# Kernel optimization log

Measured on AMD Instinct MI355X. Metric: run time of the kernel, lower is better.

## Reference

```python
import jax, jax.numpy as jnp
import numpy as np

N = 50000      # nodes per graph
E = 800000     # edges per graph
IN_DIM = 64
HIDDEN = 128
OUT_DIM = 2
P = 100000     # candidate residue pairs


def setup_inputs() -> dict:
    key = jax.random.key(0)
    ks = jax.random.split(key, 12)
    x1 = jax.random.normal(ks[0], (N, IN_DIM), dtype=jnp.float32)
    x2 = jax.random.normal(ks[1], (N, IN_DIM), dtype=jnp.float32)
    edge_index1 = jax.random.randint(ks[2], (2, E), 0, N, dtype=jnp.int64)
    edge_index2 = jax.random.randint(ks[3], (2, E), 0, N, dtype=jnp.int64)
    label = jax.random.randint(ks[4], (P, 2), 0, N, dtype=jnp.int64)
    s = 0.05
    W0 = jax.random.normal(ks[5], (IN_DIM, HIDDEN), dtype=jnp.float32) * s
    W1 = jax.random.normal(ks[6], (HIDDEN, HIDDEN), dtype=jnp.float32) * s
    W2 = jax.random.normal(ks[7], (HIDDEN, HIDDEN), dtype=jnp.float32) * s
    b0 = jnp.zeros((HIDDEN,), dtype=jnp.float32)
    b1 = jnp.zeros((HIDDEN,), dtype=jnp.float32)
    b2 = jnp.zeros((HIDDEN,), dtype=jnp.float32)
    fcW = jax.random.normal(ks[8], (2 * HIDDEN, OUT_DIM), dtype=jnp.float32) * s
    fcb = jnp.zeros((OUT_DIM,), dtype=jnp.float32)
    return {"x1": x1, "edge_index1": edge_index1, "x2": x2,
            "edge_index2": edge_index2, "label": label,
            "W0": W0, "b0": b0, "W1": W1, "b1": b1, "W2": W2, "b2": b2,
            "fcW": fcW, "fcb": fcb}


def gcn_conv(x, src, dst, W, b):
    """PyG GCNConv: linear, add self-loops, symmetric D^-1/2 (A+I) D^-1/2 aggregation."""
    n = x.shape[0]
    h = x @ W                                   # [n, out]
    loops = jnp.arange(n, dtype=src.dtype)
    src_sl = jnp.concatenate([src, loops])      # [E+n]
    dst_sl = jnp.concatenate([dst, loops])
    deg = jax.ops.segment_sum(jnp.ones_like(src_sl, dtype=h.dtype), dst_sl,
                              num_segments=n)
    dinv = jax.lax.rsqrt(jnp.maximum(deg, 1.0e-12))
    norm = dinv[src_sl] * dinv[dst_sl]          # [E+n]
    msgs = h[src_sl] * norm[:, None]            # gather + scale
    out = jax.ops.segment_sum(msgs, dst_sl, num_segments=n)  # scatter-add
    return out + b


def gcn_tower(x, edge_index, params):
    src, dst = edge_index[0], edge_index[1]
    for (W, b) in params:
        x = jax.nn.relu(gcn_conv(x, src, dst, W, b))
    return x


def reference(x1, edge_index1, x2, edge_index2, label,
              W0, b0, W1, b1, W2, b2, fcW, fcb):
    params = [(W0, b0), (W1, b1), (W2, b2)]
    x_ligand = gcn_tower(x1, edge_index1, params)    # shared GCN weights
    x_receptor = gcn_tower(x2, edge_index2, params)
    x = jnp.concatenate([x_ligand[label[:, 0]], x_receptor[label[:, 1]]], axis=1)
    return jax.nn.relu(x @ fcW + fcb)
```

## Files before the change

### kernel.cpp

```cpp
#include <hip/hip_runtime.h>
#include <math.h>

typedef __attribute__((ext_vector_type(8))) short bf16x8;
typedef __attribute__((ext_vector_type(4))) float f32x4;

__device__ inline unsigned short f2bf(float f) {
    unsigned int u = __float_as_uint(f);
    unsigned int r = u + 0x7fffu + ((u >> 16) & 1u);
    return (unsigned short)(r >> 16);
}
__device__ inline float bf2f(unsigned short b) {
    return __uint_as_float(((unsigned int)b) << 16);
}


__global__ void histU_kernel(const int* __restrict__ d1, const int* __restrict__ d2,
                             int* __restrict__ cnt, int E, int N) {
    int i = blockIdx.x * blockDim.x + threadIdx.x;
    if (i < E) atomicAdd(&cnt[d1[i]], 1);
    else if (i < 2 * E) atomicAdd(&cnt[N + d2[i - E]], 1);
}

__global__ __launch_bounds__(256) void block_reduce_kernel(const int* __restrict__ cnt,
                                                           float* __restrict__ dinv,
                                                           int* __restrict__ blockSums, int NN) {
    int i = blockIdx.x * 256 + threadIdx.x;
    int v = 0;
    if (i < NN) {
        v = cnt[i];
        dinv[i] = 1.0f / sqrtf((float)(v + 1));
    }
    int s = v;
#pragma unroll
    for (int o = 32; o; o >>= 1) s += __shfl_down(s, o);
    __shared__ int ws[4];
    if ((threadIdx.x & 63) == 0) ws[threadIdx.x >> 6] = s;
    __syncthreads();
    if (threadIdx.x == 0) blockSums[blockIdx.x] = ws[0] + ws[1] + ws[2] + ws[3];
}

__global__ __launch_bounds__(1024) void scan_sums_kernel(const int* __restrict__ blockSums,
                                                         int* __restrict__ blockOff, int nb,
                                                         int* __restrict__ rowptr, int NN) {
    __shared__ int sh[1024];
    int t = threadIdx.x;
    int v = (t < nb) ? blockSums[t] : 0;
    sh[t] = v;
    __syncthreads();
    for (int o = 1; o < 1024; o <<= 1) {
        int u = (t >= o) ? sh[t - o] : 0;
        __syncthreads();
        sh[t] += u;
        __syncthreads();
    }
    if (t < nb) blockOff[t] = sh[t] - v;
    if (t == 1023) rowptr[NN] = sh[1023];
}

__global__ __launch_bounds__(256) void scan_write_kernel(const int* __restrict__ cnt,
                                                         const int* __restrict__ blockOff,
                                                         int* __restrict__ rowptr, int NN) {
    __shared__ int sh[256];
    int i = blockIdx.x * 256 + threadIdx.x;
    int t = threadIdx.x;
    int v = (i < NN) ? cnt[i] : 0;
    sh[t] = v;
    __syncthreads();
    for (int o = 1; o < 256; o <<= 1) {
        int u = (t >= o) ? sh[t - o] : 0;
        __syncthreads();
        sh[t] += u;
        __syncthreads();
    }
    if (i < NN) rowptr[i] = blockOff[blockIdx.x] + sh[t] - v;
}

__global__ void placeU_kernel(const int* __restrict__ s1, const int* __restrict__ d1,
                              const int* __restrict__ s2, const int* __restrict__ d2,
                              const int* __restrict__ rowptr, int* __restrict__ cnt,
                              int* __restrict__ csr, int E, int N) {
    int i = blockIdx.x * blockDim.x + threadIdx.x;
    int s, d;
    if (i < E)          { s = s1[i];         d = d1[i]; }
    else if (i < 2 * E) { s = s2[i - E] + N; d = d2[i - E] + N; }
    else return;
    int p = atomicSub(&cnt[d], 1);
    csr[rowptr[d] + p - 1] = s;
}


__global__ void prep_weights(const float* __restrict__ W0, const float* __restrict__ W1,
                             const float* __restrict__ W2,
                             unsigned short* __restrict__ W0h, unsigned short* __restrict__ W0l,
                             unsigned short* __restrict__ W1h, unsigned short* __restrict__ W1l,
                             unsigned short* __restrict__ W2h, unsigned short* __restrict__ W2l) {
    const float* W; unsigned short *Wh, *Wl; int K;
    if (blockIdx.x == 0)      { W = W0; Wh = W0h; Wl = W0l; K = 64; }
    else if (blockIdx.x == 1) { W = W1; Wh = W1h; Wl = W1l; K = 128; }
    else                      { W = W2; Wh = W2h; Wl = W2l; K = 128; }
    for (int i = threadIdx.x; i < K * 128; i += 256) {
        int k = i >> 7, c = i & 127;
        float v = W[i];
        unsigned short h = f2bf(v);
        unsigned short l = f2bf(v - bf2f(h));
        Wh[c * K + k] = h;
        Wl[c * K + k] = l;
    }
}


__global__ void prescale_kernel(const float* __restrict__ x1, const float* __restrict__ x2,
                                const float* __restrict__ dinv, float* __restrict__ X0, int NN,
                                int N) {
    int i = blockIdx.x * blockDim.x + threadIdx.x;
    if (i >= NN * 16) return;
    int r = i >> 4;
    const float4* src = (r < N) ? (const float4*)(x1) + i
                                : (const float4*)(x2) + (i - N * 16);
    float4 v = *src;
    float d = dinv[r];
    v.x *= d; v.y *= d; v.z *= d; v.w *= d;
    reinterpret_cast<float4*>(X0)[i] = v;
}


__global__ void agg64_kernel(const float* __restrict__ X0, const int* __restrict__ rowptr,
                             const int* __restrict__ csr,
                             unsigned short* __restrict__ Shi, unsigned short* __restrict__ Slo,
                             int NN) {
    int w = blockIdx.x * (blockDim.x >> 6) + (threadIdx.x >> 6);
    int lane = threadIdx.x & 63;
    if (w >= NN) return;
    int beg = rowptr[w], end = rowptr[w + 1];
    float acc = X0[(size_t)w * 64 + lane];
    int e = beg;
    int full_end = beg + ((end - beg) & ~7);
    for (; e < full_end; e += 8) {
        int s0 = csr[e], s1 = csr[e + 1], s2 = csr[e + 2], s3 = csr[e + 3];
        int s4 = csr[e + 4], s5 = csr[e + 5], s6 = csr[e + 6], s7 = csr[e + 7];
        float v0 = X0[(size_t)s0 * 64 + lane];
        float v1 = X0[(size_t)s1 * 64 + lane];
        float v2 = X0[(size_t)s2 * 64 + lane];
        float v3 = X0[(size_t)s3 * 64 + lane];
        float v4 = X0[(size_t)s4 * 64 + lane];
        float v5 = X0[(size_t)s5 * 64 + lane];
        float v6 = X0[(size_t)s6 * 64 + lane];
        float v7 = X0[(size_t)s7 * 64 + lane];
        acc += ((v0 + v1) + (v2 + v3)) + ((v4 + v5) + (v6 + v7));
    }
    if (e < end) {
#pragma unroll
        for (int j = 0; j < 7; ++j) {
            int a = e + j;
            bool vld = a < end;
            int s = csr[vld ? a : beg];
            float m = vld ? 1.f : 0.f;
            acc += m * X0[(size_t)s * 64 + lane];
        }
    }
    unsigned short h = f2bf(acc);
    Shi[(size_t)w * 64 + lane] = h;
    Slo[(size_t)w * 64 + lane] = f2bf(acc - bf2f(h));
}


__global__ void agg128_kernel(const float* __restrict__ Xf, const int* __restrict__ rowptr,
                              const int* __restrict__ csr,
                              unsigned short* __restrict__ Shi, unsigned short* __restrict__ Slo,
                              int NN) {
    int w = blockIdx.x * (blockDim.x >> 6) + (threadIdx.x >> 6);
    int lane = threadIdx.x & 63;
    if (w >= NN) return;
    const float2* X = (const float2*)Xf;
    int beg = rowptr[w], end = rowptr[w + 1];
    float2 self = X[(size_t)w * 64 + lane];
    float ax = self.x, ay = self.y;
    int e = beg;
    int full_end = beg + ((end - beg) & ~7);
    for (; e < full_end; e += 8) {
        int s0 = csr[e], s1 = csr[e + 1], s2 = csr[e + 2], s3 = csr[e + 3];
        int s4 = csr[e + 4], s5 = csr[e + 5], s6 = csr[e + 6], s7 = csr[e + 7];
        float2 v0 = X[(size_t)s0 * 64 + lane];
        float2 v1 = X[(size_t)s1 * 64 + lane];
        float2 v2 = X[(size_t)s2 * 64 + lane];
        float2 v3 = X[(size_t)s3 * 64 + lane];
        float2 v4 = X[(size_t)s4 * 64 + lane];
        float2 v5 = X[(size_t)s5 * 64 + lane];
        float2 v6 = X[(size_t)s6 * 64 + lane];
        float2 v7 = X[(size_t)s7 * 64 + lane];
        ax += ((v0.x + v1.x) + (v2.x + v3.x)) + ((v4.x + v5.x) + (v6.x + v7.x));
        ay += ((v0.y + v1.y) + (v2.y + v3.y)) + ((v4.y + v5.y) + (v6.y + v7.y));
    }
    if (e < end) {
#pragma unroll
        for (int j = 0; j < 7; ++j) {
            int a = e + j;
            bool vld = a < end;
            int s = csr[vld ? a : beg];
            float m = vld ? 1.f : 0.f;
            float2 v = X[(size_t)s * 64 + lane];
            ax += m * v.x; ay += m * v.y;
        }
    }
    unsigned short hx = f2bf(ax), hy = f2bf(ay);
    ushort2 H; H.x = hx; H.y = hy;
    ushort2 L; L.x = f2bf(ax - bf2f(hx)); L.y = f2bf(ay - bf2f(hy));
    *reinterpret_cast<ushort2*>(Shi + (size_t)w * 128 + 2 * lane) = H;
    *reinterpret_cast<ushort2*>(Slo + (size_t)w * 128 + 2 * lane) = L;
}


template <int K>
__global__ __launch_bounds__(512) void gemm_mfma(const unsigned short* __restrict__ Ah,
                                                 const unsigned short* __restrict__ Al,
                                                 const unsigned short* __restrict__ WhT,
                                                 const unsigned short* __restrict__ WlT,
                                                 const float* __restrict__ bias,
                                                 const float* __restrict__ dinv, int post,
                                                 float* __restrict__ C, int M) {
    const int LDA = K + 8;
    __shared__ unsigned short ldsH[64 * LDA];
    __shared__ unsigned short ldsL[64 * LDA];

    int t = threadIdx.x;
    int lane = t & 63, wid = t >> 6;
    int c16 = lane & 15, kq = (lane >> 4) * 8;
    int row0 = blockIdx.x * 64;
    int col = wid * 16 + c16;

    bf16x8 wh[K / 32], wl[K / 32];
#pragma unroll
    for (int ks = 0; ks < K / 32; ++ks) {
        wh[ks] = *reinterpret_cast<const bf16x8*>(WhT + (size_t)col * K + ks * 32 + kq);
        wl[ks] = *reinterpret_cast<const bf16x8*>(WlT + (size_t)col * K + ks * 32 + kq);
    }

    const int CH = 64 * (K / 8);
    for (int c = t; c < CH; c += 512) {
        int row = c / (K / 8), kb = c % (K / 8);
        int gr = row0 + row; if (gr >= M) gr = M - 1;
        *reinterpret_cast<bf16x8*>(&ldsH[row * LDA + kb * 8]) =
            *reinterpret_cast<const bf16x8*>(Ah + (size_t)gr * K + kb * 8);
        *reinterpret_cast<bf16x8*>(&ldsL[row * LDA + kb * 8]) =
            *reinterpret_cast<const bf16x8*>(Al + (size_t)gr * K + kb * 8);
    }
    __syncthreads();

    float bb = bias[col];
#pragma unroll
    for (int rt = 0; rt < 4; ++rt) {
        f32x4 acc = {0.f, 0.f, 0.f, 0.f};
        int abase = (rt * 16 + c16) * LDA + kq;
#pragma unroll
        for (int ks = 0; ks < K / 32; ++ks) {
            bf16x8 ah = *reinterpret_cast<const bf16x8*>(ldsH + abase + ks * 32);
            bf16x8 al = *reinterpret_cast<const bf16x8*>(ldsL + abase + ks * 32);
            acc = __builtin_amdgcn_mfma_f32_16x16x32_bf16(ah, wh[ks], acc, 0, 0, 0);
            acc = __builtin_amdgcn_mfma_f32_16x16x32_bf16(ah, wl[ks], acc, 0, 0, 0);
            acc = __builtin_amdgcn_mfma_f32_16x16x32_bf16(al, wh[ks], acc, 0, 0, 0);
        }
#pragma unroll
        for (int r = 0; r < 4; ++r) {
            int gr = row0 + rt * 16 + (lane >> 4) * 4 + r;
            if (gr < M) {
                float d = dinv[gr];
                float po = post ? d : 1.0f;
                float v = fmaxf(acc[r] * d + bb, 0.f) * po;
                C[(size_t)gr * 128 + col] = v;
            }
        }
    }
}


__global__ void fc_kernel(const float* __restrict__ H3, const int* __restrict__ label,
                          const float* __restrict__ fcW, const float* __restrict__ fcb,
                          float* __restrict__ out, int P, int N) {
    int w = blockIdx.x * (blockDim.x >> 6) + (threadIdx.x >> 6);
    int lane = threadIdx.x & 63;
    if (w >= P) return;
    int l0 = label[2 * w], l1 = label[2 * w + 1] + N;
    float xl0 = H3[(size_t)l0 * 128 + lane];
    float xl1 = H3[(size_t)l0 * 128 + 64 + lane];
    float xr0 = H3[(size_t)l1 * 128 + lane];
    float xr1 = H3[(size_t)l1 * 128 + 64 + lane];
    float a0 = xl0 * fcW[lane * 2]             + xl1 * fcW[(64 + lane) * 2]
             + xr0 * fcW[(128 + lane) * 2]     + xr1 * fcW[(192 + lane) * 2];
    float a1 = xl0 * fcW[lane * 2 + 1]         + xl1 * fcW[(64 + lane) * 2 + 1]
             + xr0 * fcW[(128 + lane) * 2 + 1] + xr1 * fcW[(192 + lane) * 2 + 1];
#pragma unroll
    for (int o = 32; o; o >>= 1) {
        a0 += __shfl_xor(a0, o);
        a1 += __shfl_xor(a1, o);
    }
    if (lane == 0) {
        out[2 * w]     = fmaxf(a0 + fcb[0], 0.f);
        out[2 * w + 1] = fmaxf(a1 + fcb[1], 0.f);
    }
}


extern "C" void kernel_launch(void* const* d_in, const int* in_sizes, int n_in,
                              void* d_out, int out_size, void* d_ws, size_t ws_size,
                              hipStream_t stream) {
    const float* x1   = (const float*)d_in[0];
    const int*   e1   = (const int*)d_in[1];
    const float* x2   = (const float*)d_in[2];
    const int*   e2   = (const int*)d_in[3];
    const int*   label= (const int*)d_in[4];
    const float* W0   = (const float*)d_in[5];
    const float* b0   = (const float*)d_in[6];
    const float* W1   = (const float*)d_in[7];
    const float* b1   = (const float*)d_in[8];
    const float* W2   = (const float*)d_in[9];
    const float* b2   = (const float*)d_in[10];
    const float* fcW  = (const float*)d_in[11];
    const float* fcb  = (const float*)d_in[12];
    float* out = (float*)d_out;

    const int N = in_sizes[0] / 64;
    const int E = in_sizes[1] / 2;
    const int P = in_sizes[4] / 2;
    const int NN = 2 * N;
    const int NB = (NN + 255) / 256;
    const int GB = (NN + 63) / 64;

    char* ws = (char*)d_ws;
    size_t off = 0;
    auto alloc = [&](size_t bytes) -> void* {
        void* p = ws + off;
        off += (bytes + 255) & ~(size_t)255;
        return p;
    };
    int*   cnt      = (int*)alloc((size_t)NN * 4);
    int*   rowptr   = (int*)alloc((size_t)(NN + 1) * 4);
    float* dinv     = (float*)alloc((size_t)NN * 4);
    int*   csr      = (int*)alloc((size_t)2 * E * 4);
    int*   blockSums= (int*)alloc((size_t)NB * 4);
    int*   blockOff = (int*)alloc((size_t)NB * 4);
    unsigned short* Shi = (unsigned short*)alloc((size_t)NN * 128 * 2);
    unsigned short* Slo = (unsigned short*)alloc((size_t)NN * 128 * 2);
    float* Xs       = (float*)alloc((size_t)NN * 128 * 4);
    unsigned short* W0h = (unsigned short*)alloc(64 * 128 * 2);
    unsigned short* W0l = (unsigned short*)alloc(64 * 128 * 2);
    unsigned short* W1h = (unsigned short*)alloc(128 * 128 * 2);
    unsigned short* W1l = (unsigned short*)alloc(128 * 128 * 2);
    unsigned short* W2h = (unsigned short*)alloc(128 * 128 * 2);
    unsigned short* W2l = (unsigned short*)alloc(128 * 128 * 2);

    prep_weights<<<3, 256, 0, stream>>>(W0, W1, W2, W0h, W0l, W1h, W1l, W2h, W2l);

    hipMemsetAsync(cnt, 0, (size_t)NN * 4, stream);
    histU_kernel<<<(2 * E + 255) / 256, 256, 0, stream>>>(e1 + E, e2 + E, cnt, E, N);
    block_reduce_kernel<<<NB, 256, 0, stream>>>(cnt, dinv, blockSums, NN);
    scan_sums_kernel<<<1, 1024, 0, stream>>>(blockSums, blockOff, NB, rowptr, NN);
    scan_write_kernel<<<NB, 256, 0, stream>>>(cnt, blockOff, rowptr, NN);
    placeU_kernel<<<(2 * E + 255) / 256, 256, 0, stream>>>(e1, e1 + E, e2, e2 + E,
                                                           rowptr, cnt, csr, E, N);
    prescale_kernel<<<(NN * 16 + 255) / 256, 256, 0, stream>>>(x1, x2, dinv, Xs, NN, N);
    agg64_kernel<<<(NN + 3) / 4, 256, 0, stream>>>(Xs, rowptr, csr, Shi, Slo, NN);
    gemm_mfma<64><<<GB, 512, 0, stream>>>(Shi, Slo, W0h, W0l, b0, dinv, 1, Xs, NN);
    agg128_kernel<<<(NN + 3) / 4, 256, 0, stream>>>(Xs, rowptr, csr, Shi, Slo, NN);
    gemm_mfma<128><<<GB, 512, 0, stream>>>(Shi, Slo, W1h, W1l, b1, dinv, 1, Xs, NN);
    agg128_kernel<<<(NN + 3) / 4, 256, 0, stream>>>(Xs, rowptr, csr, Shi, Slo, NN);
    gemm_mfma<128><<<GB, 512, 0, stream>>>(Shi, Slo, W2h, W2l, b2, dinv, 0, Xs, NN);

    fc_kernel<<<(P + 3) / 4, 256, 0, stream>>>(Xs, label, fcW, fcb, out, P, N);
}
```

Measured before the change: 566.1 us.

## Fuse neighbor aggregation into MFMA GEMM via LDS staging

Merges each layer's CSR gather-aggregation with the following split-bf16 MFMA GEMM. Each 512-thread block aggregates its 64 rows (8 per wave) and writes the hi/lo bf16 parts straight into LDS instead of global Shi/Slo buffers. This removes the global write and re-read of the aggregated features and halves the kernel launches per layer, and ping-pong buffers avoid read/write aliasing. The trade-off is fewer waves doing the latency-bound gathers per block, plus a barrier before the MFMA phase, which may lower gather occupancy.

```diff
diff --git a/kernel.cpp b/kernel.cpp
--- a/kernel.cpp
+++ b/kernel.cpp
@@ -124,108 +124,96 @@
 }
 
 
-__global__ void agg64_kernel(const float* __restrict__ X0, const int* __restrict__ rowptr,
-                             const int* __restrict__ csr,
-                             unsigned short* __restrict__ Shi, unsigned short* __restrict__ Slo,
-                             int NN) {
-    int w = blockIdx.x * (blockDim.x >> 6) + (threadIdx.x >> 6);
-    int lane = threadIdx.x & 63;
-    if (w >= NN) return;
-    int beg = rowptr[w], end = rowptr[w + 1];
-    float acc = X0[(size_t)w * 64 + lane];
-    int e = beg;
-    int full_end = beg + ((end - beg) & ~7);
-    for (; e < full_end; e += 8) {
-        int s0 = csr[e], s1 = csr[e + 1], s2 = csr[e + 2], s3 = csr[e + 3];
-        int s4 = csr[e + 4], s5 = csr[e + 5], s6 = csr[e + 6], s7 = csr[e + 7];
-        float v0 = X0[(size_t)s0 * 64 + lane];
-        float v1 = X0[(size_t)s1 * 64 + lane];
-        float v2 = X0[(size_t)s2 * 64 + lane];
-        float v3 = X0[(size_t)s3 * 64 + lane];
-        float v4 = X0[(size_t)s4 * 64 + lane];
-        float v5 = X0[(size_t)s5 * 64 + lane];
-        float v6 = X0[(size_t)s6 * 64 + lane];
-        float v7 = X0[(size_t)s7 * 64 + lane];
-        acc += ((v0 + v1) + (v2 + v3)) + ((v4 + v5) + (v6 + v7));
-    }
-    if (e < end) {
-#pragma unroll
-        for (int j = 0; j < 7; ++j) {
-            int a = e + j;
-            bool vld = a < end;
-            int s = csr[vld ? a : beg];
-            float m = vld ? 1.f : 0.f;
-            acc += m * X0[(size_t)s * 64 + lane];
-        }
-    }
-    unsigned short h = f2bf(acc);
-    Shi[(size_t)w * 64 + lane] = h;
-    Slo[(size_t)w * 64 + lane] = f2bf(acc - bf2f(h));
-}
-
-
-__global__ void agg128_kernel(const float* __restrict__ Xf, const int* __restrict__ rowptr,
-                              const int* __restrict__ csr,
-                              unsigned short* __restrict__ Shi, unsigned short* __restrict__ Slo,
-                              int NN) {
-    int w = blockIdx.x * (blockDim.x >> 6) + (threadIdx.x >> 6);
-    int lane = threadIdx.x & 63;
-    if (w >= NN) return;
-    const float2* X = (const float2*)Xf;
-    int beg = rowptr[w], end = rowptr[w + 1];
-    float2 self = X[(size_t)w * 64 + lane];
-    float ax = self.x, ay = self.y;
-    int e = beg;
-    int full_end = beg + ((end - beg) & ~7);
-    for (; e < full_end; e += 8) {
-        int s0 = csr[e], s1 = csr[e + 1], s2 = csr[e + 2], s3 = csr[e + 3];
-        int s4 = csr[e + 4], s5 = csr[e + 5], s6 = csr[e + 6], s7 = csr[e + 7];
-        float2 v0 = X[(size_t)s0 * 64 + lane];
-        float2 v1 = X[(size_t)s1 * 64 + lane];
-        float2 v2 = X[(size_t)s2 * 64 + lane];
-        float2 v3 = X[(size_t)s3 * 64 + lane];
-        float2 v4 = X[(size_t)s4 * 64 + lane];
-        float2 v5 = X[(size_t)s5 * 64 + lane];
-        float2 v6 = X[(size_t)s6 * 64 + lane];
-        float2 v7 = X[(size_t)s7 * 64 + lane];
-        ax += ((v0.x + v1.x) + (v2.x + v3.x)) + ((v4.x + v5.x) + (v6.x + v7.x));
-        ay += ((v0.y + v1.y) + (v2.y + v3.y)) + ((v4.y + v5.y) + (v6.y + v7.y));
-    }
-    if (e < end) {
-#pragma unroll
-        for (int j = 0; j < 7; ++j) {
-            int a = e + j;
-            bool vld = a < end;
-            int s = csr[vld ? a : beg];
-            float m = vld ? 1.f : 0.f;
-            float2 v = X[(size_t)s * 64 + lane];
-            ax += m * v.x; ay += m * v.y;
-        }
-    }
-    unsigned short hx = f2bf(ax), hy = f2bf(ay);
-    ushort2 H; H.x = hx; H.y = hy;
-    ushort2 L; L.x = f2bf(ax - bf2f(hx)); L.y = f2bf(ay - bf2f(hy));
-    *reinterpret_cast<ushort2*>(Shi + (size_t)w * 128 + 2 * lane) = H;
-    *reinterpret_cast<ushort2*>(Slo + (size_t)w * 128 + 2 * lane) = L;
-}
-
-
 template <int K>
-__global__ __launch_bounds__(512) void gemm_mfma(const unsigned short* __restrict__ Ah,
-                                                 const unsigned short* __restrict__ Al,
-                                                 const unsigned short* __restrict__ WhT,
-                                                 const unsigned short* __restrict__ WlT,
-                                                 const float* __restrict__ bias,
-                                                 const float* __restrict__ dinv, int post,
-                                                 float* __restrict__ C, int M) {
+__global__ __launch_bounds__(512) void fused_agg_gemm(
+    const float* __restrict__ X, const int* __restrict__ rowptr,
+    const int* __restrict__ csr,
+    const unsigned short* __restrict__ WhT, const unsigned short* __restrict__ WlT,
+    const float* __restrict__ bias, const float* __restrict__ dinv, int post,
+    float* __restrict__ C, int M) {
     const int LDA = K + 8;
     __shared__ unsigned short ldsH[64 * LDA];
     __shared__ unsigned short ldsL[64 * LDA];
 
     int t = threadIdx.x;
     int lane = t & 63, wid = t >> 6;
+    int row0 = blockIdx.x * 64;
+
+    for (int rr = 0; rr < 8; ++rr) {
+        int row = wid * 8 + rr;
+        int g = row0 + row; if (g >= M) g = M - 1;
+        int beg = rowptr[g], end = rowptr[g + 1];
+        if constexpr (K == 128) {
+            const float2* X2 = (const float2*)X;
+            float2 self = X2[(size_t)g * 64 + lane];
+            float ax = self.x, ay = self.y;
+            int e = beg;
+            int full_end = beg + ((end - beg) & ~7);
+            for (; e < full_end; e += 8) {
+                int s0 = csr[e], s1 = csr[e + 1], s2 = csr[e + 2], s3 = csr[e + 3];
+                int s4 = csr[e + 4], s5 = csr[e + 5], s6 = csr[e + 6], s7 = csr[e + 7];
+                float2 v0 = X2[(size_t)s0 * 64 + lane];
+                float2 v1 = X2[(size_t)s1 * 64 + lane];
+                float2 v2 = X2[(size_t)s2 * 64 + lane];
+                float2 v3 = X2[(size_t)s3 * 64 + lane];
+                float2 v4 = X2[(size_t)s4 * 64 + lane];
+                float2 v5 = X2[(size_t)s5 * 64 + lane];
+                float2 v6 = X2[(size_t)s6 * 64 + lane];
+                float2 v7 = X2[(size_t)s7 * 64 + lane];
+                ax += ((v0.x + v1.x) + (v2.x + v3.x)) + ((v4.x + v5.x) + (v6.x + v7.x));
+                ay += ((v0.y + v1.y) + (v2.y + v3.y)) + ((v4.y + v5.y) + (v6.y + v7.y));
+            }
+            if (e < end) {
+#pragma unroll
+                for (int j = 0; j < 7; ++j) {
+                    int a = e + j;
+                    bool vld = a < end;
+                    int s = csr[vld ? a : beg];
+                    float m = vld ? 1.f : 0.f;
+                    float2 v = X2[(size_t)s * 64 + lane];
+                    ax += m * v.x; ay += m * v.y;
+                }
+            }
+            unsigned short hx = f2bf(ax), hy = f2bf(ay);
+            ushort2 H; H.x = hx; H.y = hy;
+            ushort2 L; L.x = f2bf(ax - bf2f(hx)); L.y = f2bf(ay - bf2f(hy));
+            *reinterpret_cast<ushort2*>(&ldsH[row * LDA + 2 * lane]) = H;
+            *reinterpret_cast<ushort2*>(&ldsL[row * LDA + 2 * lane]) = L;
+        } else {
+            float acc = X[(size_t)g * 64 + lane];
+            int e = beg;
+            int full_end = beg + ((end - beg) & ~7);
+            for (; e < full_end; e += 8) {
+                int s0 = csr[e], s1 = csr[e + 1], s2 = csr[e + 2], s3 = csr[e + 3];
+                int s4 = csr[e + 4], s5 = csr[e + 5], s6 = csr[e + 6], s7 = csr[e + 7];
+                float v0 = X[(size_t)s0 * 64 + lane];
+                float v1 = X[(size_t)s1 * 64 + lane];
+                float v2 = X[(size_t)s2 * 64 + lane];
+                float v3 = X[(size_t)s3 * 64 + lane];
+                float v4 = X[(size_t)s4 * 64 + lane];
+                float v5 = X[(size_t)s5 * 64 + lane];
+                float v6 = X[(size_t)s6 * 64 + lane];
+                float v7 = X[(size_t)s7 * 64 + lane];
+                acc += ((v0 + v1) + (v2 + v3)) + ((v4 + v5) + (v6 + v7));
+            }
+            if (e < end) {
+#pragma unroll
+                for (int j = 0; j < 7; ++j) {
+                    int a = e + j;
+                    bool vld = a < end;
+                    int s = csr[vld ? a : beg];
+                    float m = vld ? 1.f : 0.f;
+                    acc += m * X[(size_t)s * 64 + lane];
+                }
+            }
+            unsigned short h = f2bf(acc);
+            ldsH[row * LDA + lane] = h;
+            ldsL[row * LDA + lane] = f2bf(acc - bf2f(h));
+        }
+    }
+    __syncthreads();
+
     int c16 = lane & 15, kq = (lane >> 4) * 8;
-    int row0 = blockIdx.x * 64;
     int col = wid * 16 + c16;
 
     bf16x8 wh[K / 32], wl[K / 32];
@@ -234,19 +222,8 @@
         wh[ks] = *reinterpret_cast<const bf16x8*>(WhT + (size_t)col * K + ks * 32 + kq);
         wl[ks] = *reinterpret_cast<const bf16x8*>(WlT + (size_t)col * K + ks * 32 + kq);
     }
-
-    const int CH = 64 * (K / 8);
-    for (int c = t; c < CH; c += 512) {
-        int row = c / (K / 8), kb = c % (K / 8);
-        int gr = row0 + row; if (gr >= M) gr = M - 1;
-        *reinterpret_cast<bf16x8*>(&ldsH[row * LDA + kb * 8]) =
-            *reinterpret_cast<const bf16x8*>(Ah + (size_t)gr * K + kb * 8);
-        *reinterpret_cast<bf16x8*>(&ldsL[row * LDA + kb * 8]) =
-            *reinterpret_cast<const bf16x8*>(Al + (size_t)gr * K + kb * 8);
-    }
-    __syncthreads();
-
     float bb = bias[col];
+
 #pragma unroll
     for (int rt = 0; rt < 4; ++rt) {
         f32x4 acc = {0.f, 0.f, 0.f, 0.f};
@@ -338,9 +315,8 @@
     int*   csr      = (int*)alloc((size_t)2 * E * 4);
     int*   blockSums= (int*)alloc((size_t)NB * 4);
     int*   blockOff = (int*)alloc((size_t)NB * 4);
-    unsigned short* Shi = (unsigned short*)alloc((size_t)NN * 128 * 2);
-    unsigned short* Slo = (unsigned short*)alloc((size_t)NN * 128 * 2);
-    float* Xs       = (float*)alloc((size_t)NN * 128 * 4);
+    float* bufA     = (float*)alloc((size_t)NN * 128 * 4);
+    float* bufB     = (float*)alloc((size_t)NN * 128 * 4);
     unsigned short* W0h = (unsigned short*)alloc(64 * 128 * 2);
     unsigned short* W0l = (unsigned short*)alloc(64 * 128 * 2);
     unsigned short* W1h = (unsigned short*)alloc(128 * 128 * 2);
@@ -357,13 +333,13 @@
     scan_write_kernel<<<NB, 256, 0, stream>>>(cnt, blockOff, rowptr, NN);
     placeU_kernel<<<(2 * E + 255) / 256, 256, 0, stream>>>(e1, e1 + E, e2, e2 + E,
                                                            rowptr, cnt, csr, E, N);
-    prescale_kernel<<<(NN * 16 + 255) / 256, 256, 0, stream>>>(x1, x2, dinv, Xs, NN, N);
-    agg64_kernel<<<(NN + 3) / 4, 256, 0, stream>>>(Xs, rowptr, csr, Shi, Slo, NN);
-    gemm_mfma<64><<<GB, 512, 0, stream>>>(Shi, Slo, W0h, W0l, b0, dinv, 1, Xs, NN);
-    agg128_kernel<<<(NN + 3) / 4, 256, 0, stream>>>(Xs, rowptr, csr, Shi, Slo, NN);
-    gemm_mfma<128><<<GB, 512, 0, stream>>>(Shi, Slo, W1h, W1l, b1, dinv, 1, Xs, NN);
-    agg128_kernel<<<(NN + 3) / 4, 256, 0, stream>>>(Xs, rowptr, csr, Shi, Slo, NN);
-    gemm_mfma<128><<<GB, 512, 0, stream>>>(Shi, Slo, W2h, W2l, b2, dinv, 0, Xs, NN);
-
-    fc_kernel<<<(P + 3) / 4, 256, 0, stream>>>(Xs, label, fcW, fcb, out, P, N);
-}
+    prescale_kernel<<<(NN * 16 + 255) / 256, 256, 0, stream>>>(x1, x2, dinv, bufA, NN, N);
+    fused_agg_gemm<64><<<GB, 512, 0, stream>>>(bufA, rowptr, csr, W0h, W0l, b0, dinv, 1,
+                                               bufB, NN);
+    fused_agg_gemm<128><<<GB, 512, 0, stream>>>(bufB, rowptr, csr, W1h, W1l, b1, dinv, 1,
+                                                bufA, NN);
+    fused_agg_gemm<128><<<GB, 512, 0, stream>>>(bufA, rowptr, csr, W2h, W2l, b2, dinv, 0,
+                                                bufB, NN);
+
+    fc_kernel<<<(P + 3) / 4, 256, 0, stream>>>(bufB, label, fcW, fcb, out, P, N);
+}
```

Result: no change. 561.0 us (-0.9%).
